# Optimization experiments

Measured on AMD Instinct MI355X. Metric: run time of the kernel, lower is better.

Reference implementation:

```python
import jax, jax.numpy as jnp
import numpy as np

B, S, K, D = 128, 64, 10, 256
THR = -1.5


def setup_inputs() -> dict:
    key = jax.random.key(0)
    ks = jax.random.split(key, 9)
    si = 1.0 / np.sqrt(D)  # torch GRU init: U(-1/sqrt(hidden), 1/sqrt(hidden))
    u = lambda k, shape, s: jax.random.uniform(k, shape, jnp.float32, -s, s)
    return {
        "item_embs": jax.random.normal(ks[0], (B, S, K, D), jnp.float32),
        "user_embs": jax.random.normal(ks[1], (B, S, D), jnp.float32),
        "W_ih": u(ks[2], (3 * D, 2 * D), si),
        "W_hh": u(ks[3], (3 * D, D), si),
        "b_ih": u(ks[4], (3 * D,), si),
        "b_hh": u(ks[5], (3 * D,), si),
        "w_out": u(ks[6], (D,), si),
        "b_out": u(ks[7], (), si),
        "length": jax.random.randint(ks[8], (B,), 0, S),
    }


def reference(item_embs, user_embs, W_ih, W_hh, b_ih, b_hh, w_out, b_out, length):
    N = B * S
    # x['items'] = cat([item_embs.flatten(0,1), zeros_like(...)], -1)  -> [N, K, 2D]
    items_flat = item_embs.reshape(N, K, D)
    items = jnp.concatenate([items_flat, jnp.zeros_like(items_flat)], axis=-1)
    # user hidden state: gather user_embs at (length-1, clamped), repeat over S
    idx = jnp.clip(length - 1, 0, None)  # [B]
    u0 = user_embs[jnp.arange(B), idx]   # [B, D]
    h0 = jnp.repeat(u0, S, axis=0)       # [N, D]

    def gru_cell(x, h):
        gi = x @ W_ih.T + b_ih  # [N, 3D]
        gh = h @ W_hh.T + b_hh
        i_r, i_z, i_n = jnp.split(gi, 3, axis=-1)
        h_r, h_z, h_n = jnp.split(gh, 3, axis=-1)
        r = jax.nn.sigmoid(i_r + h_r)
        z = jax.nn.sigmoid(i_z + h_z)
        n = jnp.tanh(i_n + r * h_n)
        return (1.0 - z) * n + z * h

    def step(carry, x_t):
        h, mask = carry  # mask [N,1]: readout threshold gate for the click-half of input
        x = jnp.concatenate([x_t[:, :D], x_t[:, D:] * mask], axis=-1)
        h = gru_cell(x, h)
        y = h @ w_out + b_out  # [N]
        next_mask = (jax.lax.stop_gradient(y) > THR).astype(x_t.dtype)[:, None]
        return (h, next_mask), y

    xs = jnp.swapaxes(items, 0, 1)  # [K, N, 2D]
    init = (h0, jnp.ones((N, 1), item_embs.dtype))
    _, ys = jax.lax.scan(step, init, xs)  # ys [K, N]
    y = jnp.swapaxes(ys, 0, 1)  # [N, K]
    # self.w = 1, self.b = 0 -> identity calibration
    return y.reshape(B, S, K)
```

## Files before the change

kernel.cpp:

```cpp
#include <hip/hip_runtime.h>

#define BB 128
#define SS 64
#define KK 10
#define DD 256
#define NN (BB*SS)
#define ROWS 32
#define NBLK (NN/ROWS)
#define NT 1024

typedef __attribute__((ext_vector_type(8))) short short8;
typedef __attribute__((ext_vector_type(4))) float f32x4;
typedef __attribute__((ext_vector_type(4))) unsigned uint4v;

#define FRAG_ELEMS (48*8*64*8)

__device__ __forceinline__ unsigned short f2bf(float f){
  union { float f; unsigned u; } v; v.f = f;
  unsigned r = (v.u + 0x7FFFu + ((v.u >> 16) & 1u)) >> 16;
  return (unsigned short)r;
}

__device__ __forceinline__ unsigned cvtpk(float lo, float hi){
  unsigned r;
  asm("v_cvt_pk_bf16_f32 %0, %1, %2" : "=v"(r) : "v"(lo), "v"(hi));
  return r;
}

__global__ void prep_weights(const float* __restrict__ Wih,
                             const float* __restrict__ Whh,
                             unsigned short* __restrict__ fw){
  int id = blockIdx.x * 256 + threadIdx.x;
  int arr = (id >= FRAG_ELEMS);
  int r = arr ? (id - FRAG_ELEMS) : id;
  int j  = r & 7;
  int l  = (r >> 3) & 63;
  int tk = (r >> 9) & 7;
  int tn = r >> 12;
  int c  = tn * 16 + (l & 15);
  int d  = tk * 32 + ((l >> 4) << 3) + j;
  float v = arr ? Whh[c * 256 + d] : Wih[c * 512 + d];
  fw[id] = f2bf(v);
}

__global__ __launch_bounds__(NT, 4) void gru_main(
    const float* __restrict__ item, const float* __restrict__ user,
    const float* __restrict__ b_ih, const float* __restrict__ b_hh,
    const float* __restrict__ w_out, const float* __restrict__ b_out,
    const int* __restrict__ length, const unsigned short* __restrict__ ws,
    float* __restrict__ out)
{
  __shared__ unsigned short xfrag[2][2*8*64*8];
  __shared__ unsigned short hfrag[2][2*8*64*8];
  __shared__ float yp[3][16][2][4][4];

  const int tid  = threadIdx.x;
  const int lane = tid & 63;
  const int w    = tid >> 6;
  const int col  = lane & 15;
  const int q    = lane >> 4;
  const int nb   = blockIdx.x * ROWS;
  const int b    = nb / SS;
  const int sk   = blockIdx.x & 7;

  const short8* fw1 = (const short8*)ws;
  const short8* fwh = fw1 + (FRAG_ELEMS/8);

  const int d    = w*16 + col;
  const float br_  = b_ih[d]       + b_hh[d];
  const float bz_  = b_ih[256 + d] + b_hh[256 + d];
  const float bin_ = b_ih[512 + d];
  const float bhn_ = b_hh[512 + d];
  const float wo_  = w_out[d];

  const int wq0 = (w     )*512 + lane;
  const int wq1 = (16 + w)*512 + lane;
  const int wq2 = (32 + w)*512 + lane;

  int idx = length[b] - 1; if (idx < 0) idx = 0;
  const float u0 = user[((size_t)b*SS + idx)*DD + d];
  float h[2][4];
  #pragma unroll
  for (int mt = 0; mt < 2; ++mt)
    #pragma unroll
    for (int reg = 0; reg < 4; ++reg)
      h[mt][reg] = u0;

  const int tkk = d >> 5;
  const int slb = ((d >> 3) & 3) * 16;
  const int dj  = d & 7;
  {
    unsigned short hb = f2bf(u0);
    #pragma unroll
    for (int mt = 0; mt < 2; ++mt)
      #pragma unroll
      for (int reg = 0; reg < 4; ++reg)
        hfrag[0][((mt*8 + tkk)*64 + slb + q*4 + reg)*8 + dj] = hb;
  }

  const int xrow = tid >> 5;
  const int xo   = tid & 31;
  const int xmt  = xrow >> 4;
  const int xtk  = xo >> 2;
  const int xsl  = (xo & 3)*16 + (xrow & 15);
  {
    const float4* p = (const float4*)(item + ((size_t)(nb + xrow)*KK + 0)*DD + xo*8);
    float4 a0 = p[0], a1 = p[1];
    uint4v t;
    t.x = cvtpk(a0.x, a0.y); t.y = cvtpk(a0.z, a0.w);
    t.z = cvtpk(a1.x, a1.y); t.w = cvtpk(a1.z, a1.w);
    *(uint4v*)&xfrag[0][((xmt*8 + xtk)*64 + xsl)*8] = t;
  }
  __syncthreads();

  const float bout = b_out[0];

#define MFMA16(A,Bv,C) __builtin_amdgcn_mfma_f32_16x16x32_bf16(A,Bv,C,0,0,0)

  for (int k = 0; k < KK; ++k){
    const int cb  = k & 1;
    const int nbf = cb ^ 1;

    f32x4 acc[2][4];
    #pragma unroll
    for (int mt = 0; mt < 2; ++mt)
      #pragma unroll
      for (int kd = 0; kd < 4; ++kd){
        f32x4 z4 = {0.f, 0.f, 0.f, 0.f};
        acc[mt][kd] = z4;
      }

    float4 xn0, xn1;
    if (k < KK-1){
      const float4* p = (const float4*)(item + ((size_t)(nb + xrow)*KK + (k+1))*DD + xo*8);
      xn0 = p[0]; xn1 = p[1];
    }

    #pragma unroll 4
    for (int tk = 0; tk < 8; ++tk){
      const int tkv = (tk + sk) & 7;
      const int o_  = tkv * 64;
      short8 w1r = fw1[wq0+o_], w1z = fw1[wq1+o_], w1n = fw1[wq2+o_];
      short8 whr = fwh[wq0+o_], whz = fwh[wq1+o_], whn = fwh[wq2+o_];
      short8 ax0 = *(const short8*)&xfrag[cb][((    tkv)*64 + lane)*8];
      short8 ax1 = *(const short8*)&xfrag[cb][((8 + tkv)*64 + lane)*8];
      short8 ah0 = *(const short8*)&hfrag[cb][((    tkv)*64 + lane)*8];
      short8 ah1 = *(const short8*)&hfrag[cb][((8 + tkv)*64 + lane)*8];
      __builtin_amdgcn_s_setprio(1);
      acc[0][0] = MFMA16(ax0, w1r, acc[0][0]);
      acc[0][0] = MFMA16(ah0, whr, acc[0][0]);
      acc[0][1] = MFMA16(ax0, w1z, acc[0][1]);
      acc[0][1] = MFMA16(ah0, whz, acc[0][1]);
      acc[0][2] = MFMA16(ax0, w1n, acc[0][2]);
      acc[0][3] = MFMA16(ah0, whn, acc[0][3]);
      acc[1][0] = MFMA16(ax1, w1r, acc[1][0]);
      acc[1][0] = MFMA16(ah1, whr, acc[1][0]);
      acc[1][1] = MFMA16(ax1, w1z, acc[1][1]);
      acc[1][1] = MFMA16(ah1, whz, acc[1][1]);
      acc[1][2] = MFMA16(ax1, w1n, acc[1][2]);
      acc[1][3] = MFMA16(ah1, whn, acc[1][3]);
      __builtin_amdgcn_s_setprio(0);
    }

    float ypl[2][4];
    #pragma unroll
    for (int mt = 0; mt < 2; ++mt)
      #pragma unroll
      for (int reg = 0; reg < 4; ++reg){
        float rp = acc[mt][0][reg] + br_;
        float zp = acc[mt][1][reg] + bz_;
        float r  = __builtin_amdgcn_rcpf(1.f + __expf(-rp));
        float z  = __builtin_amdgcn_rcpf(1.f + __expf(-zp));
        float np = acc[mt][2][reg] + bin_ + r*(acc[mt][3][reg] + bhn_);
        np = __builtin_amdgcn_fmed3f(np, -30.f, 30.f);
        float e  = __expf(2.f*np);
        float n  = 1.f - 2.f*__builtin_amdgcn_rcpf(e + 1.f);
        float hv = (1.f - z)*n + z*h[mt][reg];
        h[mt][reg] = hv;
        ypl[mt][reg] = hv * wo_;
      }

    #pragma unroll
    for (int mt = 0; mt < 2; ++mt)
      #pragma unroll
      for (int reg = 0; reg < 4; ++reg){
        float p = ypl[mt][reg];
        p += __shfl_xor(p, 1);
        p += __shfl_xor(p, 2);
        p += __shfl_xor(p, 4);
        p += __shfl_xor(p, 8);
        if (col == 0) yp[k % 3][w][mt][q][reg] = p;
      }

    #pragma unroll
    for (int mt = 0; mt < 2; ++mt)
      #pragma unroll
      for (int reg = 0; reg < 4; ++reg)
        hfrag[nbf][((mt*8 + tkk)*64 + slb + q*4 + reg)*8 + dj] = f2bf(h[mt][reg]);

    if (k < KK-1){
      uint4v t;
      t.x = cvtpk(xn0.x, xn0.y); t.y = cvtpk(xn0.z, xn0.w);
      t.z = cvtpk(xn1.x, xn1.y); t.w = cvtpk(xn1.z, xn1.w);
      *(uint4v*)&xfrag[nbf][((xmt*8 + xtk)*64 + xsl)*8] = t;
    }

    if (k > 0 && tid < 32){
      float s = bout;
      #pragma unroll
      for (int ww = 0; ww < 16; ++ww)
        s += yp[(k-1) % 3][ww][tid >> 4][(tid >> 2) & 3][tid & 3];
      out[(size_t)(nb + tid)*KK + (k-1)] = s;
    }

    asm volatile("s_waitcnt lgkmcnt(0)" ::: "memory");
    __builtin_amdgcn_s_barrier();
    __builtin_amdgcn_sched_barrier(0);
  }

  if (tid < 32){
    float s = bout;
    #pragma unroll
    for (int ww = 0; ww < 16; ++ww)
      s += yp[(KK-1) % 3][ww][tid >> 4][(tid >> 2) & 3][tid & 3];
    out[(size_t)(nb + tid)*KK + (KK-1)] = s;
  }
}

extern "C" void kernel_launch(void* const* d_in, const int* in_sizes, int n_in,
                              void* d_out, int out_size, void* d_ws, size_t ws_size,
                              hipStream_t stream) {
  const float* item   = (const float*)d_in[0];
  const float* user   = (const float*)d_in[1];
  const float* W_ih   = (const float*)d_in[2];
  const float* W_hh   = (const float*)d_in[3];
  const float* b_ih   = (const float*)d_in[4];
  const float* b_hh   = (const float*)d_in[5];
  const float* w_out  = (const float*)d_in[6];
  const float* b_out  = (const float*)d_in[7];
  const int*   length = (const int*)d_in[8];
  unsigned short* ws  = (unsigned short*)d_ws;
  float* out = (float*)d_out;

  hipLaunchKernelGGL(prep_weights, dim3((2*FRAG_ELEMS)/256), dim3(256), 0, stream,
                     W_ih, W_hh, ws);
  hipLaunchKernelGGL(gru_main, dim3(NBLK), dim3(NT), 0, stream,
                     item, user, b_ih, b_hh, w_out, b_out, length, ws, out);
}
```

Before: 220.4 us.

## Batch input-projection GEMM across two timesteps to reuse W_ih fragment loads

Splits each GRU step into an input-projection part and a recurrent part. The x@W_ih products for two consecutive timesteps are computed together, once per pair of steps, so each W_ih fragment fetched from global memory feeds twice as many MFMAs. The recurrent h@W_hh part stays per step. Item inputs for the next pair of steps are prefetched and staged into both x buffers at the end of the pair. The cost is a dozen extra live accumulator vectors across the pair, which raises register pressure at 1024 threads per block.

```diff
diff --git a/kernel.cpp b/kernel.cpp
--- a/kernel.cpp
+++ b/kernel.cpp
@@ -103,13 +103,14 @@
   const int xmt  = xrow >> 4;
   const int xtk  = xo >> 2;
   const int xsl  = (xo & 3)*16 + (xrow & 15);
-  {
-    const float4* p = (const float4*)(item + ((size_t)(nb + xrow)*KK + 0)*DD + xo*8);
+  #pragma unroll
+  for (int s = 0; s < 2; ++s){
+    const float4* p = (const float4*)(item + ((size_t)(nb + xrow)*KK + s)*DD + xo*8);
     float4 a0 = p[0], a1 = p[1];
     uint4v t;
     t.x = cvtpk(a0.x, a0.y); t.y = cvtpk(a0.z, a0.w);
     t.z = cvtpk(a1.x, a1.y); t.w = cvtpk(a1.z, a1.w);
-    *(uint4v*)&xfrag[0][((xmt*8 + xtk)*64 + xsl)*8] = t;
+    *(uint4v*)&xfrag[s][((xmt*8 + xtk)*64 + xsl)*8] = t;
   }
   __syncthreads();
 
@@ -117,105 +118,140 @@
 
 #define MFMA16(A,Bv,C) __builtin_amdgcn_mfma_f32_16x16x32_bf16(A,Bv,C,0,0,0)
 
-  for (int k = 0; k < KK; ++k){
-    const int cb  = k & 1;
-    const int nbf = cb ^ 1;
-
-    f32x4 acc[2][4];
-    #pragma unroll
-    for (int mt = 0; mt < 2; ++mt)
-      #pragma unroll
-      for (int kd = 0; kd < 4; ++kd){
-        f32x4 z4 = {0.f, 0.f, 0.f, 0.f};
-        acc[mt][kd] = z4;
-      }
-
-    float4 xn0, xn1;
-    if (k < KK-1){
-      const float4* p = (const float4*)(item + ((size_t)(nb + xrow)*KK + (k+1))*DD + xo*8);
-      xn0 = p[0]; xn1 = p[1];
-    }
-
-    #pragma unroll 4
+  for (int c = 0; c < KK/2; ++c){
+    f32x4 gi[2][2][3];
+    #pragma unroll
+    for (int s = 0; s < 2; ++s)
+      #pragma unroll
+      for (int mt = 0; mt < 2; ++mt)
+        #pragma unroll
+        for (int g = 0; g < 3; ++g){
+          f32x4 z4 = {0.f, 0.f, 0.f, 0.f};
+          gi[s][mt][g] = z4;
+        }
+
+    #pragma unroll 2
     for (int tk = 0; tk < 8; ++tk){
       const int tkv = (tk + sk) & 7;
       const int o_  = tkv * 64;
       short8 w1r = fw1[wq0+o_], w1z = fw1[wq1+o_], w1n = fw1[wq2+o_];
-      short8 whr = fwh[wq0+o_], whz = fwh[wq1+o_], whn = fwh[wq2+o_];
-      short8 ax0 = *(const short8*)&xfrag[cb][((    tkv)*64 + lane)*8];
-      short8 ax1 = *(const short8*)&xfrag[cb][((8 + tkv)*64 + lane)*8];
-      short8 ah0 = *(const short8*)&hfrag[cb][((    tkv)*64 + lane)*8];
-      short8 ah1 = *(const short8*)&hfrag[cb][((8 + tkv)*64 + lane)*8];
+      short8 a00 = *(const short8*)&xfrag[0][((    tkv)*64 + lane)*8];
+      short8 a01 = *(const short8*)&xfrag[0][((8 + tkv)*64 + lane)*8];
+      short8 a10 = *(const short8*)&xfrag[1][((    tkv)*64 + lane)*8];
+      short8 a11 = *(const short8*)&xfrag[1][((8 + tkv)*64 + lane)*8];
       __builtin_amdgcn_s_setprio(1);
-      acc[0][0] = MFMA16(ax0, w1r, acc[0][0]);
-      acc[0][0] = MFMA16(ah0, whr, acc[0][0]);
-      acc[0][1] = MFMA16(ax0, w1z, acc[0][1]);
-      acc[0][1] = MFMA16(ah0, whz, acc[0][1]);
-      acc[0][2] = MFMA16(ax0, w1n, acc[0][2]);
-      acc[0][3] = MFMA16(ah0, whn, acc[0][3]);
-      acc[1][0] = MFMA16(ax1, w1r, acc[1][0]);
-      acc[1][0] = MFMA16(ah1, whr, acc[1][0]);
-      acc[1][1] = MFMA16(ax1, w1z, acc[1][1]);
-      acc[1][1] = MFMA16(ah1, whz, acc[1][1]);
-      acc[1][2] = MFMA16(ax1, w1n, acc[1][2]);
-      acc[1][3] = MFMA16(ah1, whn, acc[1][3]);
+      gi[0][0][0] = MFMA16(a00, w1r, gi[0][0][0]);
+      gi[0][0][1] = MFMA16(a00, w1z, gi[0][0][1]);
+      gi[0][0][2] = MFMA16(a00, w1n, gi[0][0][2]);
+      gi[0][1][0] = MFMA16(a01, w1r, gi[0][1][0]);
+      gi[0][1][1] = MFMA16(a01, w1z, gi[0][1][1]);
+      gi[0][1][2] = MFMA16(a01, w1n, gi[0][1][2]);
+      gi[1][0][0] = MFMA16(a10, w1r, gi[1][0][0]);
+      gi[1][0][1] = MFMA16(a10, w1z, gi[1][0][1]);
+      gi[1][0][2] = MFMA16(a10, w1n, gi[1][0][2]);
+      gi[1][1][0] = MFMA16(a11, w1r, gi[1][1][0]);
+      gi[1][1][1] = MFMA16(a11, w1z, gi[1][1][1]);
+      gi[1][1][2] = MFMA16(a11, w1n, gi[1][1][2]);
       __builtin_amdgcn_s_setprio(0);
     }
 
-    float ypl[2][4];
-    #pragma unroll
-    for (int mt = 0; mt < 2; ++mt)
-      #pragma unroll
-      for (int reg = 0; reg < 4; ++reg){
-        float rp = acc[mt][0][reg] + br_;
-        float zp = acc[mt][1][reg] + bz_;
-        float r  = __builtin_amdgcn_rcpf(1.f + __expf(-rp));
-        float z  = __builtin_amdgcn_rcpf(1.f + __expf(-zp));
-        float np = acc[mt][2][reg] + bin_ + r*(acc[mt][3][reg] + bhn_);
-        np = __builtin_amdgcn_fmed3f(np, -30.f, 30.f);
-        float e  = __expf(2.f*np);
-        float n  = 1.f - 2.f*__builtin_amdgcn_rcpf(e + 1.f);
-        float hv = (1.f - z)*n + z*h[mt][reg];
-        h[mt][reg] = hv;
-        ypl[mt][reg] = hv * wo_;
-      }
-
-    #pragma unroll
-    for (int mt = 0; mt < 2; ++mt)
-      #pragma unroll
-      for (int reg = 0; reg < 4; ++reg){
-        float p = ypl[mt][reg];
-        p += __shfl_xor(p, 1);
-        p += __shfl_xor(p, 2);
-        p += __shfl_xor(p, 4);
-        p += __shfl_xor(p, 8);
-        if (col == 0) yp[k % 3][w][mt][q][reg] = p;
-      }
-
-    #pragma unroll
-    for (int mt = 0; mt < 2; ++mt)
-      #pragma unroll
-      for (int reg = 0; reg < 4; ++reg)
-        hfrag[nbf][((mt*8 + tkk)*64 + slb + q*4 + reg)*8 + dj] = f2bf(h[mt][reg]);
-
-    if (k < KK-1){
-      uint4v t;
-      t.x = cvtpk(xn0.x, xn0.y); t.y = cvtpk(xn0.z, xn0.w);
-      t.z = cvtpk(xn1.x, xn1.y); t.w = cvtpk(xn1.z, xn1.w);
-      *(uint4v*)&xfrag[nbf][((xmt*8 + xtk)*64 + xsl)*8] = t;
+    #pragma unroll
+    for (int s = 0; s < 2; ++s){
+      const int k   = 2*c + s;
+      const int cb  = s;
+      const int nbf = s ^ 1;
+
+      f32x4 acc[2][3];
+      #pragma unroll
+      for (int mt = 0; mt < 2; ++mt){
+        acc[mt][0] = gi[s][mt][0];
+        acc[mt][1] = gi[s][mt][1];
+        f32x4 z4 = {0.f, 0.f, 0.f, 0.f};
+        acc[mt][2] = z4;
+      }
+
+      float4 xa0, xa1, xb0, xb1;
+      if (s == 1 && c < KK/2-1){
+        const float4* pA = (const float4*)(item + ((size_t)(nb + xrow)*KK + (2*c+2))*DD + xo*8);
+        const float4* pB = (const float4*)(item + ((size_t)(nb + xrow)*KK + (2*c+3))*DD + xo*8);
+        xa0 = pA[0]; xa1 = pA[1]; xb0 = pB[0]; xb1 = pB[1];
+      }
+
+      #pragma unroll 4
+      for (int tk = 0; tk < 8; ++tk){
+        const int tkv = (tk + sk) & 7;
+        const int o_  = tkv * 64;
+        short8 whr = fwh[wq0+o_], whz = fwh[wq1+o_], whn = fwh[wq2+o_];
+        short8 ah0 = *(const short8*)&hfrag[cb][((    tkv)*64 + lane)*8];
+        short8 ah1 = *(const short8*)&hfrag[cb][((8 + tkv)*64 + lane)*8];
+        __builtin_amdgcn_s_setprio(1);
+        acc[0][0] = MFMA16(ah0, whr, acc[0][0]);
+        acc[0][1] = MFMA16(ah0, whz, acc[0][1]);
+        acc[0][2] = MFMA16(ah0, whn, acc[0][2]);
+        acc[1][0] = MFMA16(ah1, whr, acc[1][0]);
+        acc[1][1] = MFMA16(ah1, whz, acc[1][1]);
+        acc[1][2] = MFMA16(ah1, whn, acc[1][2]);
+        __builtin_amdgcn_s_setprio(0);
+      }
+
+      float ypl[2][4];
+      #pragma unroll
+      for (int mt = 0; mt < 2; ++mt)
+        #pragma unroll
+        for (int reg = 0; reg < 4; ++reg){
+          float rp = acc[mt][0][reg] + br_;
+          float zp = acc[mt][1][reg] + bz_;
+          float r  = __builtin_amdgcn_rcpf(1.f + __expf(-rp));
+          float z  = __builtin_amdgcn_rcpf(1.f + __expf(-zp));
+          float np = gi[s][mt][2][reg] + bin_ + r*(acc[mt][2][reg] + bhn_);
+          np = __builtin_amdgcn_fmed3f(np, -30.f, 30.f);
+          float e  = __expf(2.f*np);
+          float n  = 1.f - 2.f*__builtin_amdgcn_rcpf(e + 1.f);
+          float hv = (1.f - z)*n + z*h[mt][reg];
+          h[mt][reg] = hv;
+          ypl[mt][reg] = hv * wo_;
+        }
+
+      #pragma unroll
+      for (int mt = 0; mt < 2; ++mt)
+        #pragma unroll
+        for (int reg = 0; reg < 4; ++reg){
+          float p = ypl[mt][reg];
+          p += __shfl_xor(p, 1);
+          p += __shfl_xor(p, 2);
+          p += __shfl_xor(p, 4);
+          p += __shfl_xor(p, 8);
+          if (col == 0) yp[k % 3][w][mt][q][reg] = p;
+        }
+
+      #pragma unroll
+      for (int mt = 0; mt < 2; ++mt)
+        #pragma unroll
+        for (int reg = 0; reg < 4; ++reg)
+          hfrag[nbf][((mt*8 + tkk)*64 + slb + q*4 + reg)*8 + dj] = f2bf(h[mt][reg]);
+
+      if (s == 1 && c < KK/2-1){
+        uint4v t;
+        t.x = cvtpk(xa0.x, xa0.y); t.y = cvtpk(xa0.z, xa0.w);
+        t.z = cvtpk(xa1.x, xa1.y); t.w = cvtpk(xa1.z, xa1.w);
+        *(uint4v*)&xfrag[0][((xmt*8 + xtk)*64 + xsl)*8] = t;
+        t.x = cvtpk(xb0.x, xb0.y); t.y = cvtpk(xb0.z, xb0.w);
+        t.z = cvtpk(xb1.x, xb1.y); t.w = cvtpk(xb1.z, xb1.w);
+        *(uint4v*)&xfrag[1][((xmt*8 + xtk)*64 + xsl)*8] = t;
+      }
+
+      if (k > 0 && tid < 32){
+        float sacc = bout;
+        #pragma unroll
+        for (int ww = 0; ww < 16; ++ww)
+          sacc += yp[(k-1) % 3][ww][tid >> 4][(tid >> 2) & 3][tid & 3];
+        out[(size_t)(nb + tid)*KK + (k-1)] = sacc;
+      }
+
+      asm volatile("s_waitcnt lgkmcnt(0)" ::: "memory");
+      __builtin_amdgcn_s_barrier();
+      __builtin_amdgcn_sched_barrier(0);
     }
-
-    if (k > 0 && tid < 32){
-      float s = bout;
-      #pragma unroll
-      for (int ww = 0; ww < 16; ++ww)
-        s += yp[(k-1) % 3][ww][tid >> 4][(tid >> 2) & 3][tid & 3];
-      out[(size_t)(nb + tid)*KK + (k-1)] = s;
-    }
-
-    asm volatile("s_waitcnt lgkmcnt(0)" ::: "memory");
-    __builtin_amdgcn_s_barrier();
-    __builtin_amdgcn_sched_barrier(0);
   }
 
   if (tid < 32){
```

New measurement: 217.5 us, median of 2. No clear change (-1.3%).
